# Performance work log

Measured on AMD Instinct MI355X. Metric: run time of the kernel, lower is better.

## Reference

```python
import jax, jax.numpy as jnp
import numpy as np

HIDDEN = 2048
FFN = 1408          # moe_inter_padding_size
NUM_EXPERTS = 8
TOP_K = 2
SEQ = 4096


def setup_inputs() -> dict:
    key = jax.random.key(0)
    k1, k2, k3, k4 = jax.random.split(key, 4)
    hidden_states = jax.random.normal(k1, (SEQ, HIDDEN), dtype=jnp.float32)
    gate_w = jax.random.normal(k2, (HIDDEN, NUM_EXPERTS), dtype=jnp.float32) * 0.02
    # fused gate+up projection per expert: [E, 2*FFN, HIDDEN]
    w1 = jax.random.normal(k3, (NUM_EXPERTS, 2 * FFN, HIDDEN), dtype=jnp.float32) * 0.02
    # down projection per expert: [E, HIDDEN, FFN]
    w2 = jax.random.normal(k4, (NUM_EXPERTS, HIDDEN, FFN), dtype=jnp.float32) * 0.02
    return {"hidden_states": hidden_states, "gate_w": gate_w, "w1": w1, "w2": w2}


def reference(hidden_states, gate_w, w1, w2):
    seq, hidden = hidden_states.shape
    # --- router ---
    router_logits = hidden_states @ gate_w                 # [T, E]
    probs = jax.nn.softmax(router_logits.astype(jnp.float32), axis=-1)
    topk_vals, topk_idx = jax.lax.top_k(probs, TOP_K)      # [T, k]
    routing_weights = topk_vals / jnp.sum(topk_vals, axis=-1, keepdims=True)
    # combine matrix [T, E]: weight of expert e for token t (0 if not selected)
    t_ids = jnp.arange(seq)[:, None]
    combine = jnp.zeros((seq, NUM_EXPERTS), dtype=jnp.float32)
    combine = combine.at[t_ids, topk_idx].add(routing_weights)
    # --- experts (dense-per-expert reference of the fused grouped GEMM) ---
    # h: [E, T, 2F]
    h = jnp.einsum('th,efh->etf', hidden_states, w1)
    g, u = jnp.split(h, 2, axis=-1)                        # SiLU-gated MLP
    act = jax.nn.silu(g) * u                               # [E, T, F]
    y = jnp.einsum('etf,ehf->eth', act, w2)                # [E, T, H]
    final_hidden_states = jnp.einsum('te,eth->th', combine, y).astype(hidden_states.dtype)
    return final_hidden_states, router_logits
```

## Files before the change

### kernel.cpp

```cpp
#include <hip/hip_runtime.h>
#include <math.h>

#define T_SEQ 4096
#define HID 2048
#define FFN1 1408
#define TWO_FFN 2816
#define NE 8
#define NSLOT 8192
#define MAXT 72

typedef unsigned short u16;
typedef __bf16 bf16x8_t __attribute__((ext_vector_type(8)));
typedef float f32x4_t __attribute__((ext_vector_type(4)));

__device__ __forceinline__ u16 f2bf(float f) {
    union { float f; unsigned int u; } v; v.f = f;
    unsigned int u = v.u;
    unsigned int r = u + 0x7FFFu + ((u >> 16) & 1u);
    return (u16)(r >> 16);
}
__device__ __forceinline__ float bf2f(u16 b) {
    union { unsigned int u; float f; } v; v.u = ((unsigned int)b) << 16;
    return v.f;
}
__device__ __forceinline__ unsigned pack2(float a, float b) {
    return (unsigned)f2bf(a) | ((unsigned)f2bf(b) << 16);
}

__global__ __launch_bounds__(256) void cvt_kernel(const float* __restrict__ in,
                                                  u16* __restrict__ out, long n) {
    long i = ((long)blockIdx.x * 256 + threadIdx.x) * 8;
    if (i + 8 > n) return;
    const float4* p = (const float4*)(in + i);
    float4 a = p[0], b = p[1];
    uint4 o;
    o.x = pack2(a.x, a.y);
    o.y = pack2(a.z, a.w);
    o.z = pack2(b.x, b.y);
    o.w = pack2(b.z, b.w);
    *(uint4*)(out + i) = o;
}

__global__ __launch_bounds__(256) void router_kernel(
    const float* __restrict__ x, const float* __restrict__ gw,
    float* __restrict__ logits_out, int* __restrict__ pairs,
    float2* __restrict__ wts, int* __restrict__ counts) {
    int wave = threadIdx.x >> 6, lane = threadIdx.x & 63;
    int t = blockIdx.x * 4 + wave;
    float acc[NE] = {0.f,0.f,0.f,0.f,0.f,0.f,0.f,0.f};
    const float* xr = x + (long)t * HID;
    for (int i = 0; i < HID / 64; ++i) {
        int hh = i * 64 + lane;
        float xv = xr[hh];
        const float4* g4 = (const float4*)(gw + (long)hh * NE);
        float4 g0 = g4[0], g1 = g4[1];
        acc[0] += xv * g0.x; acc[1] += xv * g0.y;
        acc[2] += xv * g0.z; acc[3] += xv * g0.w;
        acc[4] += xv * g1.x; acc[5] += xv * g1.y;
        acc[6] += xv * g1.z; acc[7] += xv * g1.w;
    }
    #pragma unroll
    for (int m = 1; m < 64; m <<= 1) {
        #pragma unroll
        for (int e = 0; e < NE; ++e) acc[e] += __shfl_xor(acc[e], m, 64);
    }
    if (lane == 0) {
        float* lo = logits_out + (long)t * NE;
        #pragma unroll
        for (int e = 0; e < NE; ++e) lo[e] = acc[e];
        int a = 0; float va = acc[0];
        #pragma unroll
        for (int e = 1; e < NE; ++e) if (acc[e] > va) { va = acc[e]; a = e; }
        int b = -1; float vb = 0.f;
        #pragma unroll
        for (int e = 0; e < NE; ++e) {
            if (e == a) continue;
            if (b < 0 || acc[e] > vb) { vb = acc[e]; b = e; }
        }
        float w0 = 1.0f / (1.0f + expf(vb - va));
        pairs[t] = a | (b << 8);
        wts[t] = make_float2(w0, 1.0f - w0);
        atomicAdd(counts + a, 1);
        atomicAdd(counts + b, 1);
    }
}

__global__ void offsets_kernel(const int* __restrict__ counts, int* __restrict__ offs,
                               int* __restrict__ tiles) {
    int s = 0;
    for (int e = 0; e < NE; ++e) { offs[e] = s; s += counts[e]; }
    offs[NE] = s;
    int nt = 0;
    for (int e = 0; e < NE; ++e)
        for (int m0 = 0; m0 < counts[e]; m0 += 128)
            tiles[nt++] = (e << 20) | m0;
    for (; nt < MAXT; ++nt) tiles[nt] = -1;
}

__global__ __launch_bounds__(256) void scatter_kernel(
    const int* __restrict__ pairs, const int* __restrict__ offs,
    int* __restrict__ cursor, int* __restrict__ tok_of, int* __restrict__ inv) {
    int t = blockIdx.x * 256 + threadIdx.x;
    if (t >= T_SEQ) return;
    int pr = pairs[t];
    int a = pr & 0xFF, b = (pr >> 8) & 0xFF;
    int p0 = atomicAdd(cursor + a, 1);
    int s0 = offs[a] + p0;
    tok_of[s0] = t; inv[2 * t] = s0;
    int p1 = atomicAdd(cursor + b, 1);
    int s1 = offs[b] + p1;
    tok_of[s1] = t; inv[2 * t + 1] = s1;
}

__global__ __launch_bounds__(256) void gather_kernel(
    const float* __restrict__ x, const int* __restrict__ tok_of, u16* __restrict__ Ab) {
    int slot = blockIdx.x;
    int tok = tok_of[slot];
    int c = threadIdx.x * 8;
    const float4* p = (const float4*)(x + (long)tok * HID + c);
    float4 a = p[0], b = p[1];
    uint4 o;
    o.x = pack2(a.x, a.y);
    o.y = pack2(a.z, a.w);
    o.z = pack2(b.x, b.y);
    o.w = pack2(b.z, b.w);
    *(uint4*)(Ab + (long)slot * HID + c) = o;
}

__device__ __forceinline__ void async16(const u16* g, u16* l) {
    __builtin_amdgcn_global_load_lds(
        (const __attribute__((address_space(1))) void*)g,
        (__attribute__((address_space(3))) void*)l, 16, 0, 0);
}

__global__ __launch_bounds__(256) void gemm_bt(
    const u16* __restrict__ A, const u16* __restrict__ B, u16* __restrict__ C,
    const int* __restrict__ offs, const int* __restrict__ tiles,
    int N, int K, int ldc, int Mtot) {
    int ent = tiles[blockIdx.x];
    if (ent < 0) return;
    int e = ent >> 20;
    int m0 = ent & 0xFFFFF;
    int m_base = offs[e];
    int m_cnt = offs[e + 1] - m_base;
    int n0 = blockIdx.y * 128;

    __shared__ u16 As[2 * 128 * 32];
    __shared__ u16 Bs[2 * 128 * 32];

    int tid = threadIdx.x;
    int lane = tid & 63;
    int wave = tid >> 6;
    const u16* Be = B + (long)e * N * K;

    int rA0 = m_base + m0 + (tid >> 2);
    int rA1 = rA0 + 64;
    if (rA0 > Mtot - 1) rA0 = Mtot - 1;
    if (rA1 > Mtot - 1) rA1 = Mtot - 1;
    int ch = (tid & 3) * 8;
    const u16* gA0 = A + (long)rA0 * K + ch;
    const u16* gA1 = A + (long)rA1 * K + ch;
    const u16* gB0 = Be + (long)(n0 + (tid >> 2)) * K + ch;
    const u16* gB1 = Be + (long)(n0 + 64 + (tid >> 2)) * K + ch;

    f32x4_t acc[4][4] = {};
    int wm = (wave >> 1) << 6;
    int wn = (wave & 1) << 6;
    int fr = lane & 15;
    int kg = (lane >> 4) * 8;

    async16(gA0, As + tid * 8);
    async16(gA1, As + (256 + tid) * 8);
    async16(gB0, Bs + tid * 8);
    async16(gB1, Bs + (256 + tid) * 8);

    int p = 0;
    for (int k0 = 0; k0 < K; k0 += 32) {
        __syncthreads();
        int kn = k0 + 32;
        if (kn < K) {
            int q = p ^ 1;
            async16(gA0 + kn, As + q * 4096 + tid * 8);
            async16(gA1 + kn, As + q * 4096 + (256 + tid) * 8);
            async16(gB0 + kn, Bs + q * 4096 + tid * 8);
            async16(gB1 + kn, Bs + q * 4096 + (256 + tid) * 8);
        }
        const u16* Ap = As + p * 4096;
        const u16* Bp = Bs + p * 4096;
        bf16x8_t av[4], bv[4];
        #pragma unroll
        for (int i = 0; i < 4; ++i)
            av[i] = *(const bf16x8_t*)(Ap + (wm + i * 16 + fr) * 32 + kg);
        #pragma unroll
        for (int j = 0; j < 4; ++j)
            bv[j] = *(const bf16x8_t*)(Bp + (wn + j * 16 + fr) * 32 + kg);
        #pragma unroll
        for (int i = 0; i < 4; ++i)
            #pragma unroll
            for (int j = 0; j < 4; ++j)
                acc[i][j] = __builtin_amdgcn_mfma_f32_16x16x32_bf16(av[i], bv[j], acc[i][j], 0, 0, 0);
        p ^= 1;
    }

    int cr = (lane >> 4) * 4;
    int cc = lane & 15;
    #pragma unroll
    for (int i = 0; i < 4; ++i) {
        #pragma unroll
        for (int j = 0; j < 4; ++j) {
            int gcol = n0 + wn + j * 16 + cc;
            #pragma unroll
            for (int r = 0; r < 4; ++r) {
                int mr = m0 + wm + i * 16 + cr + r;
                if (mr < m_cnt)
                    C[(long)(m_base + mr) * ldc + gcol] = f2bf(acc[i][j][r]);
            }
        }
    }
}

__global__ __launch_bounds__(256) void act_kernel(const u16* __restrict__ h,
                                                  u16* __restrict__ act) {
    long i = (long)blockIdx.x * 256 + threadIdx.x;
    long s = i / (FFN1 / 4);
    int f = (int)(i % (FFN1 / 4)) * 4;
    const u16* hr = h + s * TWO_FFN;
    uint2 gv = *(const uint2*)(hr + f);
    uint2 uv = *(const uint2*)(hr + FFN1 + f);
    float g0 = bf2f((u16)(gv.x & 0xFFFF)), g1 = bf2f((u16)(gv.x >> 16));
    float g2 = bf2f((u16)(gv.y & 0xFFFF)), g3 = bf2f((u16)(gv.y >> 16));
    float u0 = bf2f((u16)(uv.x & 0xFFFF)), u1 = bf2f((u16)(uv.x >> 16));
    float u2 = bf2f((u16)(uv.y & 0xFFFF)), u3 = bf2f((u16)(uv.y >> 16));
    float a0 = g0 / (1.f + expf(-g0)) * u0;
    float a1 = g1 / (1.f + expf(-g1)) * u1;
    float a2 = g2 / (1.f + expf(-g2)) * u2;
    float a3 = g3 / (1.f + expf(-g3)) * u3;
    uint2 o;
    o.x = pack2(a0, a1);
    o.y = pack2(a2, a3);
    *(uint2*)(act + s * FFN1 + f) = o;
}

__global__ __launch_bounds__(256) void combine_kernel(
    const u16* __restrict__ y, const int* __restrict__ inv,
    const float2* __restrict__ wts, float* __restrict__ out) {
    int t = blockIdx.x >> 1;
    int c = ((blockIdx.x & 1) << 10) + threadIdx.x * 4;
    int s0 = inv[2 * t], s1 = inv[2 * t + 1];
    float2 w = wts[t];
    uint2 a = *(const uint2*)(y + (long)s0 * HID + c);
    uint2 b = *(const uint2*)(y + (long)s1 * HID + c);
    float4 o;
    o.x = w.x * bf2f((u16)(a.x & 0xFFFF)) + w.y * bf2f((u16)(b.x & 0xFFFF));
    o.y = w.x * bf2f((u16)(a.x >> 16))   + w.y * bf2f((u16)(b.x >> 16));
    o.z = w.x * bf2f((u16)(a.y & 0xFFFF)) + w.y * bf2f((u16)(b.y & 0xFFFF));
    o.w = w.x * bf2f((u16)(a.y >> 16))   + w.y * bf2f((u16)(b.y >> 16));
    *(float4*)(out + (long)t * HID + c) = o;
}

extern "C" void kernel_launch(void* const* d_in, const int* in_sizes, int n_in,
                              void* d_out, int out_size, void* d_ws, size_t ws_size,
                              hipStream_t stream) {
    const float* hidden = (const float*)d_in[0];
    const float* gate_w = (const float*)d_in[1];
    const float* w1     = (const float*)d_in[2];
    const float* w2     = (const float*)d_in[3];
    float* out_final  = (float*)d_out;
    float* out_logits = out_final + (long)T_SEQ * HID;

    const long W1N = (long)NE * TWO_FFN * HID;
    const long W2N = (long)NE * HID * FFN1;
    const long ABN = (long)NSLOT * HID;
    const long HN  = (long)NSLOT * TWO_FFN;

    u16* w1b = (u16*)d_ws;
    u16* w2b = w1b + W1N;
    u16* Ab  = w2b + W2N;
    u16* h   = Ab + ABN;
    int* counts = (int*)(h + HN);
    int* cursor = counts + 8;
    int* offs   = counts + 16;
    int* pairs  = counts + 32;
    float2* wts = (float2*)(pairs + T_SEQ);
    int* tok_of = (int*)(wts + T_SEQ);
    int* inv    = tok_of + NSLOT;
    int* tiles  = inv + 2 * T_SEQ;
    u16* act = w1b;
    u16* yb  = Ab;

    hipMemsetAsync(counts, 0, 64, stream);
    router_kernel<<<T_SEQ / 4, 256, 0, stream>>>(hidden, gate_w, out_logits, pairs, wts, counts);
    offsets_kernel<<<1, 1, 0, stream>>>(counts, offs, tiles);
    scatter_kernel<<<T_SEQ / 256, 256, 0, stream>>>(pairs, offs, cursor, tok_of, inv);
    gather_kernel<<<NSLOT, 256, 0, stream>>>(hidden, tok_of, Ab);
    cvt_kernel<<<(int)(W1N / 2048), 256, 0, stream>>>(w1, w1b, W1N);
    cvt_kernel<<<(int)(W2N / 2048), 256, 0, stream>>>(w2, w2b, W2N);
    gemm_bt<<<dim3(MAXT, TWO_FFN / 128), 256, 0, stream>>>(Ab, w1b, h, offs, tiles, TWO_FFN, HID, TWO_FFN, NSLOT);
    act_kernel<<<(int)((long)NSLOT * FFN1 / 4 / 256), 256, 0, stream>>>(h, act);
    gemm_bt<<<dim3(MAXT, HID / 128), 256, 0, stream>>>(act, w2b, yb, offs, tiles, HID, FFN1, HID, NSLOT);
    combine_kernel<<<NSLOT, 256, 0, stream>>>(yb, inv, wts, out_final);
}
```

Before: 793.5 us.

## Swizzle GEMM shared-memory K-chunks and parallelize offsets with wave scan

The GEMM now XOR-swizzles which 8-element K chunk each thread loads into shared memory and which chunk each MFMA lane reads. This is meant to spread accesses across LDS banks and cut bank conflicts on the 32-wide tile rows. Separately, the single-thread offsets kernel becomes a 64-lane wave that builds expert offsets and the tile list with shuffle-based prefix scans. The swizzle must match between the store and read patterns, or the GEMM results will be wrong.

```diff
diff --git a/kernel.cpp b/kernel.cpp
--- a/kernel.cpp
+++ b/kernel.cpp
@@ -87,14 +87,29 @@
 
 __global__ void offsets_kernel(const int* __restrict__ counts, int* __restrict__ offs,
                                int* __restrict__ tiles) {
-    int s = 0;
-    for (int e = 0; e < NE; ++e) { offs[e] = s; s += counts[e]; }
-    offs[NE] = s;
-    int nt = 0;
-    for (int e = 0; e < NE; ++e)
-        for (int m0 = 0; m0 < counts[e]; m0 += 128)
-            tiles[nt++] = (e << 20) | m0;
-    for (; nt < MAXT; ++nt) tiles[nt] = -1;
+    int lane = threadIdx.x;
+    int c = (lane < NE) ? counts[lane] : 0;
+    int s = c;
+    #pragma unroll
+    for (int m = 1; m < NE; m <<= 1) {
+        int t = __shfl_up(s, m, 64);
+        if (lane >= m) s += t;
+    }
+    if (lane < NE) offs[lane] = s - c;
+    if (lane == NE - 1) offs[NE] = s;
+    int nt = (lane < NE) ? ((c + 127) >> 7) : 0;
+    int ts = nt;
+    #pragma unroll
+    for (int m = 1; m < NE; m <<= 1) {
+        int t = __shfl_up(ts, m, 64);
+        if (lane >= m) ts += t;
+    }
+    int tbase = ts - nt;
+    if (lane < NE)
+        for (int i = 0; i < nt; ++i) tiles[tbase + i] = (lane << 20) | (i << 7);
+    int nt_tot = __shfl(ts, NE - 1, 64);
+    for (int j = lane; j < MAXT; j += 64)
+        if (j >= nt_tot) tiles[j] = -1;
 }
 
 __global__ __launch_bounds__(256) void scatter_kernel(
@@ -157,7 +172,7 @@
     int rA1 = rA0 + 64;
     if (rA0 > Mtot - 1) rA0 = Mtot - 1;
     if (rA1 > Mtot - 1) rA1 = Mtot - 1;
-    int ch = (tid & 3) * 8;
+    int ch = ((tid & 3) ^ ((tid >> 3) & 3)) * 8;
     const u16* gA0 = A + (long)rA0 * K + ch;
     const u16* gA1 = A + (long)rA1 * K + ch;
     const u16* gB0 = Be + (long)(n0 + (tid >> 2)) * K + ch;
@@ -167,7 +182,7 @@
     int wm = (wave >> 1) << 6;
     int wn = (wave & 1) << 6;
     int fr = lane & 15;
-    int kg = (lane >> 4) * 8;
+    int kg = ((lane >> 4) ^ ((lane >> 1) & 3)) * 8;
 
     async16(gA0, As + tid * 8);
     async16(gA1, As + (256 + tid) * 8);
@@ -290,7 +305,7 @@
 
     hipMemsetAsync(counts, 0, 64, stream);
     router_kernel<<<T_SEQ / 4, 256, 0, stream>>>(hidden, gate_w, out_logits, pairs, wts, counts);
-    offsets_kernel<<<1, 1, 0, stream>>>(counts, offs, tiles);
+    offsets_kernel<<<1, 64, 0, stream>>>(counts, offs, tiles);
     scatter_kernel<<<T_SEQ / 256, 256, 0, stream>>>(pairs, offs, cursor, tok_of, inv);
     gather_kernel<<<NSLOT, 256, 0, stream>>>(hidden, tok_of, Ab);
     cvt_kernel<<<(int)(W1N / 2048), 256, 0, stream>>>(w1, w1b, W1N);
```

Result: no change. 784.0 us (-1.2%).
